# Kernel optimization log

Hardware: AMD Instinct MI355X
Metric: run time of the kernel (lower is better)

## Reference

```python
import jax, jax.numpy as jnp
import numpy as np

B, D, H, U, K = 256, 512, 512, 24, 8
IK, IV, NIH = 64, 400, 1          # input attention: key/query 64, value 400, 1 head
CK, CQ, NCH = 32, 32, 4           # comm attention: key/query 32, 4 heads
CV = H                            # comm_value_size forced to hidden_size in __init__
_SQ_IK = np.float32(np.sqrt(IK))
_SQ_CK = np.float32(np.sqrt(CK))


def setup_inputs() -> dict:
    key = jax.random.key(0)
    ks = jax.random.split(key, 12)
    n = jax.random.normal
    s = jnp.float32(0.02)
    return {
        "x": n(ks[0], (B, 1, D), jnp.float32),
        "hs": n(ks[1], (B, U, H), jnp.float32),
        "cs": n(ks[2], (B, U, H), jnp.float32),
        "key_w": n(ks[3], (D, NIH * IK)) * s,
        "key_b": jnp.zeros((NIH * IK,), jnp.float32),
        "value_w": n(ks[4], (D, NIH * IV)) * s,
        "value_b": jnp.zeros((NIH * IV,), jnp.float32),
        "query_w": n(ks[5], (U, H, NIH * IK)) * s,
        "i2h_w": n(ks[6], (U, IV, 4 * H)) * s,
        "h2h_w": n(ks[7], (U, H, 4 * H)) * s,
        "qc_w": n(ks[8], (U, H, NCH * CQ)) * s,
        "kc_w": n(ks[9], (U, H, NCH * CK)) * s,
        "vc_w": n(ks[10], (U, H, NCH * CV)) * s,
        "co_w": n(ks[11], (U, NCH * CV, CV)) * s,
    }


def _forward(x, hs, cs, key_w, key_b, value_w, value_b, query_w,
             i2h_w, h2h_w, qc_w, kc_w, vc_w, co_w):
    b = x.shape[0]
    # append null input -> [B,2,D]
    xx = jnp.concatenate([x, jnp.zeros_like(x)], axis=1)
    # ---- input attention + top-k unit selection ----
    k_lay = (xx @ key_w + key_b).reshape(b, 2, NIH, IK).transpose(0, 2, 1, 3)    # [B,NIH,2,IK]
    v_lay = (xx @ value_w + value_b).reshape(b, 2, NIH, IV).mean(axis=2)         # [B,2,IV] (mean over heads)
    q_lay = jnp.einsum('buh,uhk->buk', hs, query_w).reshape(b, U, NIH, IK).transpose(0, 2, 1, 3)
    scores = jnp.einsum('bnuk,bntk->bnut', q_lay, k_lay) / _SQ_IK               # [B,NIH,U,2]
    scores = scores.mean(axis=1)                                                 # [B,U,2]
    _, idx = jax.lax.top_k(scores[:, :, 0], K)                                   # top-k on not-null score
    mask = jnp.zeros((b, U), x.dtype).at[jnp.arange(b)[:, None], idx].set(1.0)   # [B,U]
    probs = jax.nn.softmax(scores, axis=-1)                                      # dropout off (eval)
    inp = jnp.einsum('but,btv->buv', probs, v_lay) * mask[:, :, None]            # [B,U,IV]
    # ---- block LSTM (GroupLSTMCell) ----
    preact = (jnp.einsum('buv,uvh->buh', inp, i2h_w)
              + jnp.einsum('buh,uhg->bug', hs, h2h_w))                           # [B,U,4H]
    i_t = jax.nn.sigmoid(preact[..., :H])
    f_t = jax.nn.sigmoid(preact[..., H:2 * H])
    o_t = jax.nn.sigmoid(preact[..., 2 * H:3 * H])
    g_t = jnp.tanh(preact[..., 3 * H:])
    c_t = cs * f_t + i_t * g_t
    h_t = o_t * jnp.tanh(c_t)
    m3 = mask[:, :, None]
    # blocked_grad: identity forward, grad*mask backward
    h_blk = h_t * m3 + jax.lax.stop_gradient(h_t * (1.0 - m3))
    # ---- multi-head communication attention ----
    qc = jnp.einsum('buh,uhk->buk', h_blk, qc_w).reshape(b, U, NCH, CQ).transpose(0, 2, 1, 3)
    kc = jnp.einsum('buh,uhk->buk', h_blk, kc_w).reshape(b, U, NCH, CK).transpose(0, 2, 1, 3)
    vc = jnp.einsum('buh,uhk->buk', h_blk, vc_w).reshape(b, U, NCH, CV).transpose(0, 2, 1, 3)
    att = jax.nn.softmax(jnp.einsum('bnuk,bntk->bnut', qc, kc) / _SQ_CK, axis=-1)
    att = att * mask[:, None, :, None]                                           # mask query rows
    ctx = jnp.einsum('bnut,bntv->bnuv', att, vc).transpose(0, 2, 1, 3).reshape(b, U, NCH * CV)
    ctx = jnp.einsum('bud,udh->buh', ctx, co_w) + h_blk
    # ---- masked state update ----
    hs_new = m3 * ctx + (1.0 - m3) * hs
    cs_new = m3 * c_t + (1.0 - m3) * cs
    return hs_new, cs_new


def reference(x, hs, cs, key_w, key_b, value_w, value_b, query_w,
              i2h_w, h2h_w, qc_w, kc_w, vc_w, co_w):
    return _forward(x, hs, cs, key_w, key_b, value_w, value_b, query_w,
                    i2h_w, h2h_w, qc_w, kc_w, vc_w, co_w)
```

## Files before the change

### kernel.cpp

```cpp
#include <hip/hip_runtime.h>


typedef unsigned short u16;
typedef __bf16 bf16_t;
typedef bf16_t bf16x8 __attribute__((ext_vector_type(8)));
typedef float f32x16 __attribute__((ext_vector_type(16)));

union V8 { uint4 u; bf16x8 v; u16 us[8]; };

__device__ __forceinline__ float u2f(u16 u) {
    union { unsigned int i; float f; } c; c.i = ((unsigned int)u) << 16; return c.f;
}
__device__ __forceinline__ u16 f2u(float f) {
    union { bf16_t b; u16 u; } c; c.b = (bf16_t)f; return c.u;
}

__global__ __launch_bounds__(256) void kv_kernel(
    const float* __restrict__ x, const float* __restrict__ key_w, const float* __restrict__ key_b,
    const float* __restrict__ value_w, const float* __restrict__ value_b,
    float* __restrict__ k0, float* __restrict__ v0)
{
    __shared__ float xs[512];
    const int b = blockIdx.x, tid = threadIdx.x;
    for (int i = tid; i < 512; i += 256) xs[i] = x[b * 512 + i];
    __syncthreads();
    if (tid < 64) {
        float acc = 0.f;
        for (int d = 0; d < 512; ++d) acc += xs[d] * key_w[d * 64 + tid];
        k0[b * 64 + tid] = acc + key_b[tid];
    }
    for (int v = tid; v < 400; v += 256) {
        float acc = 0.f;
        for (int d = 0; d < 512; ++d) acc += xs[d] * value_w[d * 400 + v];
        v0[b * 400 + v] = acc + value_b[v];
    }
}

__global__ __launch_bounds__(64) void qscore_kernel(
    const float* __restrict__ hs, const float* __restrict__ query_w,
    const float* __restrict__ k0, const float* __restrict__ key_b,
    float* __restrict__ scores)
{
    __shared__ float hsu[512];
    const int u = blockIdx.x, b = blockIdx.y, lane = threadIdx.x;
    const float* h = hs + ((size_t)(b * 24 + u)) * 512;
    for (int i = lane; i < 512; i += 64) hsu[i] = h[i];
    __syncthreads();
    const float* qw = query_w + (size_t)u * 512 * 64 + lane;
    float q = 0.f;
    for (int d = 0; d < 512; ++d) q += hsu[d] * qw[(size_t)d * 64];
    float p0 = q * k0[b * 64 + lane];
    float p1 = q * key_b[lane];
    #pragma unroll
    for (int off = 32; off > 0; off >>= 1) {
        p0 += __shfl_down(p0, off);
        p1 += __shfl_down(p1, off);
    }
    if (lane == 0) {
        scores[(b * 24 + u) * 2 + 0] = p0 * 0.125f;
        scores[(b * 24 + u) * 2 + 1] = p1 * 0.125f;
    }
}

__global__ __launch_bounds__(64) void topk_kernel(
    const float* __restrict__ scores, float* __restrict__ mask, float* __restrict__ probs)
{
    __shared__ float s0[24];
    const int b = blockIdx.x, tid = threadIdx.x;
    if (tid < 24) s0[tid] = scores[(b * 24 + tid) * 2];
    __syncthreads();
    if (tid < 24) {
        const float su = s0[tid];
        int rank = 0;
        for (int t = 0; t < 24; ++t) {
            float st = s0[t];
            rank += (st > su) || (st == su && t < tid);
        }
        mask[b * 24 + tid] = (rank < 8) ? 1.f : 0.f;
        const float a = su, c = scores[(b * 24 + tid) * 2 + 1];
        const float m = fmaxf(a, c);
        const float e0 = expf(a - m), e1 = expf(c - m);
        const float inv = 1.f / (e0 + e1);
        probs[(b * 24 + tid) * 2 + 0] = e0 * inv;
        probs[(b * 24 + tid) * 2 + 1] = e1 * inv;
    }
}

__global__ __launch_bounds__(256) void inp_kernel(
    const float* __restrict__ probs, const float* __restrict__ v0,
    const float* __restrict__ value_b, const float* __restrict__ mask,
    u16* __restrict__ inp)
{
    const int idx = blockIdx.x * 256 + threadIdx.x;
    const int v = idx % 416, bu = idx / 416, b = bu / 24;
    float val = 0.f;
    if (v < 400)
        val = (probs[bu * 2] * v0[b * 400 + v] + probs[bu * 2 + 1] * value_b[v]) * mask[bu];
    inp[idx] = f2u(val);
}

__global__ __launch_bounds__(256) void tobf16_kernel(
    const float* __restrict__ src, u16* __restrict__ dst)
{
    const int idx = blockIdx.x * 256 + threadIdx.x;
    dst[idx] = f2u(src[idx]);
}

__device__ __forceinline__ void gemm_pipe(
    const u16* __restrict__ aB1, int lda1,
    const float* __restrict__ bB1, int ldb1, int K1, int ns1,
    const u16* __restrict__ aB2, int lda2,
    const float* __restrict__ bB2, int ldb2, int K2, int ns2,
    int ar, int ac, int bn, int bkg, int wm, int wn, int fr, int kh,
    u16* __restrict__ As0, u16* __restrict__ As1,
    u16* __restrict__ Bs0, u16* __restrict__ Bs1,
    f32x16 acc[2][2])
{
    const int nst = ns1 + ns2;
    uint4 a0A, a1A, a0B, a1B;
    float rbA[16], rbB[16];

    auto issue = [&](int t, uint4& x0, uint4& x1, float* rb) {
        const bool s2 = (t >= ns1);
        const int k0 = (s2 ? t - ns1 : t) << 5;
        const int lda = s2 ? lda2 : lda1;
        const int ldb = s2 ? ldb2 : ldb1;
        const int K   = s2 ? K2 : K1;
        const u16* ap = (s2 ? aB2 : aB1) + k0;
        x0 = *(const uint4*)ap;
        x1 = *(const uint4*)(ap + (size_t)64 * lda);
        const float* bp = (s2 ? bB2 : bB1) + (size_t)k0 * ldb;
        if (k0 + 32 <= K) {
            #pragma unroll
            for (int j = 0; j < 16; ++j) rb[j] = bp[(size_t)j * ldb];
        } else {
            #pragma unroll
            for (int j = 0; j < 16; ++j)
                rb[j] = (k0 + bkg + j < K) ? bp[(size_t)j * ldb] : 0.f;
        }
    };

    auto convstore = [&](const uint4& x0, const uint4& x1, const float* rb,
                         u16* __restrict__ As, u16* __restrict__ Bs) {
        *(uint4*)&As[ar * 40 + ac]        = x0;
        *(uint4*)&As[(ar + 64) * 40 + ac] = x1;
        V8 lo, hi;
        #pragma unroll
        for (int j = 0; j < 8; ++j) lo.us[j] = f2u(rb[j]);
        #pragma unroll
        for (int j = 0; j < 8; ++j) hi.us[j] = f2u(rb[8 + j]);
        *(uint4*)&Bs[bn * 40 + bkg]     = lo.u;
        *(uint4*)&Bs[bn * 40 + bkg + 8] = hi.u;
    };

    auto compute = [&](const u16* __restrict__ As, const u16* __restrict__ Bs) {
        #pragma unroll
        for (int kk = 0; kk < 32; kk += 16) {
            V8 a0, a1, b0, b1;
            a0.u = *(const uint4*)&As[(wm + fr) * 40 + kk + kh];
            a1.u = *(const uint4*)&As[(wm + 32 + fr) * 40 + kk + kh];
            b0.u = *(const uint4*)&Bs[(wn + fr) * 40 + kk + kh];
            b1.u = *(const uint4*)&Bs[(wn + 32 + fr) * 40 + kk + kh];
            acc[0][0] = __builtin_amdgcn_mfma_f32_32x32x16_bf16(a0.v, b0.v, acc[0][0], 0, 0, 0);
            acc[0][1] = __builtin_amdgcn_mfma_f32_32x32x16_bf16(a0.v, b1.v, acc[0][1], 0, 0, 0);
            acc[1][0] = __builtin_amdgcn_mfma_f32_32x32x16_bf16(a1.v, b0.v, acc[1][0], 0, 0, 0);
            acc[1][1] = __builtin_amdgcn_mfma_f32_32x32x16_bf16(a1.v, b1.v, acc[1][1], 0, 0, 0);
        }
    };

    issue(0, a0A, a1A, rbA);
    convstore(a0A, a1A, rbA, As0, Bs0);
    if (nst > 1) issue(1, a0B, a1B, rbB);
    __syncthreads();

    for (int t = 0; t < nst; t += 2) {
        compute(As0, Bs0);
        if (t + 1 < nst) convstore(a0B, a1B, rbB, As1, Bs1);
        if (t + 2 < nst) issue(t + 2, a0A, a1A, rbA);
        __syncthreads();
        if (t + 1 < nst) {
            compute(As1, Bs1);
            if (t + 2 < nst) convstore(a0A, a1A, rbA, As0, Bs0);
            if (t + 3 < nst) issue(t + 3, a0B, a1B, rbB);
            __syncthreads();
        }
    }
}

__global__ __launch_bounds__(256, 2) void mfma_gemm(
    const u16* __restrict__ A1, int lda1, int aus1,
    const float* __restrict__ B1, int ldb1, int bus1, int K1,
    const u16* __restrict__ A2, int lda2, int aus2,
    const float* __restrict__ B2, int ldb2, int bus2, int K2,
    void* __restrict__ Cv, int ldc, int cus, int mode,
    int skA, int skB, int skC)
{
    __shared__ __align__(16) u16 As[2][128 * 40];
    __shared__ __align__(16) u16 Bs[2][128 * 40];
    const int u = blockIdx.z;
    const int n0 = blockIdx.x * 128;
    const int mb = blockIdx.y & 1, sk = blockIdx.y >> 1;
    const int m0 = mb * 128;
    const int tid = threadIdx.x;
    const int ar = tid >> 2, ac = (tid & 3) * 8;
    const int bn = tid & 127, bkg = (tid >> 7) * 16;
    const int w = tid >> 6, lane = tid & 63;
    const int wm = (w >> 1) * 64, wn = (w & 1) * 64;
    const int fr = lane & 31, kh = (lane >> 5) * 8;

    const int ns1 = (K1 + 31) >> 5;
    const int ns2 = K2 ? (K2 + 31) >> 5 : 0;

    const u16* aB1 = A1 + (size_t)sk * skA + (size_t)u * aus1 + (size_t)(m0 + ar) * lda1 + ac;
    const float* bB1 = B1 + (size_t)sk * skB + (size_t)u * bus1 + (size_t)bkg * ldb1 + n0 + bn;
    const u16* aB2 = aB1; const float* bB2 = bB1; int lda2e = lda1, ldb2e = ldb1;
    if (K2) {
        aB2 = A2 + (size_t)u * aus2 + (size_t)(m0 + ar) * lda2 + ac;
        bB2 = B2 + (size_t)u * bus2 + (size_t)bkg * ldb2 + n0 + bn;
        lda2e = lda2; ldb2e = ldb2;
    }

    f32x16 acc[2][2];
    #pragma unroll
    for (int i = 0; i < 2; ++i)
        #pragma unroll
        for (int j = 0; j < 2; ++j)
            #pragma unroll
            for (int r = 0; r < 16; ++r) acc[i][j][r] = 0.f;

    gemm_pipe(aB1, lda1, bB1, ldb1, K1, ns1,
              aB2, lda2e, bB2, ldb2e, K2, ns2,
              ar, ac, bn, bkg, wm, wn, fr, kh,
              As[0], As[1], Bs[0], Bs[1], acc);

    const size_t skoff = (size_t)sk * (size_t)skC;
    const int rbase = (lane >> 5) * 4;
    #pragma unroll
    for (int i = 0; i < 2; ++i) {
        #pragma unroll
        for (int j = 0; j < 2; ++j) {
            const int gn = n0 + wn + j * 32 + fr;
            #pragma unroll
            for (int r = 0; r < 16; ++r) {
                const int row = (r & 3) + 8 * (r >> 2) + rbase;
                const int gm = m0 + wm + i * 32 + row;
                const size_t idx = (size_t)u * cus + (size_t)gm * ldc + gn + skoff;
                if (mode == 0) ((float*)Cv)[idx] = acc[i][j][r];
                else           ((u16*)Cv)[idx]  = f2u(acc[i][j][r]);
            }
        }
    }
}

__global__ __launch_bounds__(256, 2) void mfma_gemm_kqv(
    const u16* __restrict__ ht,
    const float* __restrict__ kc_w, const float* __restrict__ qc_w, const float* __restrict__ vc_w,
    u16* __restrict__ kc, u16* __restrict__ qcb, u16* __restrict__ vc)
{
    __shared__ __align__(16) u16 As[2][128 * 40];
    __shared__ __align__(16) u16 Bs[2][128 * 40];
    const int u = blockIdx.z;
    const int bx = blockIdx.x;
    const int m0 = blockIdx.y * 128;
    const int tid = threadIdx.x;
    const int ar = tid >> 2, ac = (tid & 3) * 8;
    const int bn = tid & 127, bkg = (tid >> 7) * 16;
    const int w = tid >> 6, lane = tid & 63;
    const int wm = (w >> 1) * 64, wn = (w & 1) * 64;
    const int fr = lane & 31, kh = (lane >> 5) * 8;

    const float* Bw; u16* Cd; int ldb, bus, n0, ldc, cus;
    if (bx == 0)      { Bw = kc_w; Cd = kc;  ldb = 128;  bus = 512 * 128;  n0 = 0;              ldc = 3072;  cus = 128;  }
    else if (bx == 1) { Bw = qc_w; Cd = qcb; ldb = 128;  bus = 512 * 128;  n0 = 0;              ldc = 3072;  cus = 128;  }
    else              { Bw = vc_w; Cd = vc;  ldb = 2048; bus = 512 * 2048; n0 = (bx - 2) * 128; ldc = 49152; cus = 2048; }

    const u16* aB = ht + (size_t)u * 512 + (size_t)(m0 + ar) * 12288 + ac;
    const float* bB = Bw + (size_t)u * bus + (size_t)bkg * ldb + n0 + bn;

    f32x16 acc[2][2];
    #pragma unroll
    for (int i = 0; i < 2; ++i)
        #pragma unroll
        for (int j = 0; j < 2; ++j)
            #pragma unroll
            for (int r = 0; r < 16; ++r) acc[i][j][r] = 0.f;

    gemm_pipe(aB, 12288, bB, ldb, 512, 16,
              aB, 12288, bB, ldb, 0, 0,
              ar, ac, bn, bkg, wm, wn, fr, kh,
              As[0], As[1], Bs[0], Bs[1], acc);

    const int rbase = (lane >> 5) * 4;
    #pragma unroll
    for (int i = 0; i < 2; ++i) {
        #pragma unroll
        for (int j = 0; j < 2; ++j) {
            const int gn = n0 + wn + j * 32 + fr;
            #pragma unroll
            for (int r = 0; r < 16; ++r) {
                const int row = (r & 3) + 8 * (r >> 2) + rbase;
                const int gm = m0 + wm + i * 32 + row;
                Cd[(size_t)u * cus + (size_t)gm * ldc + gn] = f2u(acc[i][j][r]);
            }
        }
    }
}

__global__ __launch_bounds__(256) void gates_kernel(
    const float* __restrict__ preact, const float* __restrict__ cs,
    const float* __restrict__ mask,
    u16* __restrict__ ht, float* __restrict__ out_cs)
{
    const int idx = blockIdx.x * 256 + threadIdx.x;
    const int h = idx & 511, bu = idx >> 9;
    const float* pre = preact + (size_t)bu * 2048;
    const float it = 1.f / (1.f + expf(-pre[h]));
    const float ft = 1.f / (1.f + expf(-pre[512 + h]));
    const float ot = 1.f / (1.f + expf(-pre[1024 + h]));
    const float gt = tanhf(pre[1536 + h]);
    const float c = cs[idx] * ft + it * gt;
    ht[idx] = f2u(ot * tanhf(c));
    out_cs[idx] = (mask[bu] != 0.f) ? c : cs[idx];
}

__global__ __launch_bounds__(64) void attn_kernel(
    const u16* __restrict__ qc, const u16* __restrict__ kc, const u16* __restrict__ vc,
    const float* __restrict__ mask, u16* __restrict__ ctx)
{
    const int u = blockIdx.x, nc = blockIdx.y, b = blockIdx.z;
    if (mask[b * 24 + u] == 0.f) return;
    const int lane = threadIdx.x;
    __shared__ float kcs[24][32];
    __shared__ float qv[32];
    __shared__ float ss[24];
    __shared__ float ps[24];
    for (int i = lane; i < 24 * 32; i += 64) {
        const int t = i >> 5, k = i & 31;
        kcs[t][k] = u2f(kc[((size_t)(b * 24 + t)) * 128 + nc * 32 + k]);
    }
    if (lane < 32) qv[lane] = u2f(qc[((size_t)(b * 24 + u)) * 128 + nc * 32 + lane]);
    __syncthreads();
    if (lane < 24) {
        float s = 0.f;
        for (int k = 0; k < 32; ++k) s += qv[k] * kcs[lane][k];
        ss[lane] = s * 0.17677669529663687f;
    }
    __syncthreads();
    float m = -1e30f;
    for (int t = 0; t < 24; ++t) m = fmaxf(m, ss[t]);
    float sum = 0.f;
    for (int t = 0; t < 24; ++t) sum += expf(ss[t] - m);
    const float inv = 1.f / sum;
    if (lane < 24) ps[lane] = expf(ss[lane] - m) * inv;
    __syncthreads();
    float acc[8] = {};
    const u16* vcb = vc + (size_t)b * 24 * 2048 + nc * 512 + lane;
    for (int t = 0; t < 24; ++t) {
        const float pt = ps[t];
        const u16* vr = vcb + (size_t)t * 2048;
        #pragma unroll
        for (int j = 0; j < 8; ++j) acc[j] += pt * u2f(vr[j * 64]);
    }
    u16* cb = ctx + ((size_t)(b * 24 + u)) * 2048 + nc * 512 + lane;
    #pragma unroll
    for (int j = 0; j < 8; ++j) cb[j * 64] = f2u(acc[j]);
}

__global__ __launch_bounds__(256) void co_reduce(
    const float* __restrict__ p, const float* __restrict__ mask,
    const u16* __restrict__ ht, const float* __restrict__ hs,
    float* __restrict__ out_hs)
{
    const int idx = blockIdx.x * 256 + threadIdx.x;
    const int bu = idx >> 9;
    out_hs[idx] = (mask[bu] != 0.f)
        ? (p[idx] + p[idx + 6144 * 512] + u2f(ht[idx]))
        : hs[idx];
}

extern "C" void kernel_launch(void* const* d_in, const int* in_sizes, int n_in,
                              void* d_out, int out_size, void* d_ws, size_t ws_size,
                              hipStream_t stream)
{
    (void)in_sizes; (void)n_in; (void)out_size; (void)ws_size;
    const float* x       = (const float*)d_in[0];
    const float* hs      = (const float*)d_in[1];
    const float* cs      = (const float*)d_in[2];
    const float* key_w   = (const float*)d_in[3];
    const float* key_b   = (const float*)d_in[4];
    const float* value_w = (const float*)d_in[5];
    const float* value_b = (const float*)d_in[6];
    const float* query_w = (const float*)d_in[7];
    const float* i2h_w   = (const float*)d_in[8];
    const float* h2h_w   = (const float*)d_in[9];
    const float* qc_w    = (const float*)d_in[10];
    const float* kc_w    = (const float*)d_in[11];
    const float* vc_w    = (const float*)d_in[12];
    const float* co_w    = (const float*)d_in[13];

    char* ws = (char*)d_ws;
    float* k0     = (float*)(ws + 0);
    float* v0     = (float*)(ws + 65536);
    float* scores = (float*)(ws + 475136);
    float* probs  = (float*)(ws + 524288);
    float* mask   = (float*)(ws + 573440);
    u16*   inp    = (u16*)  (ws + 598016);
    float* preact = (float*)(ws + 5709824);
    u16*   vc     = (u16*)  (ws + 5709824);
    float* co_p   = (float*)(ws + 5709824);
    u16*   ctx    = (u16*)  (ws + 30875648);
    u16*   ht     = (u16*)  (ws + 56041472);
    u16*   kc     = (u16*)  (ws + 62332928);
    u16*   qcb    = (u16*)  (ws + 63905792);
    u16*   hsb    = (u16*)  (ws + 65478656);

    float* out_hs = (float*)d_out;
    float* out_cs = out_hs + (size_t)256 * 24 * 512;

    kv_kernel<<<256, 256, 0, stream>>>(x, key_w, key_b, value_w, value_b, k0, v0);
    qscore_kernel<<<dim3(24, 256), 64, 0, stream>>>(hs, query_w, k0, key_b, scores);
    topk_kernel<<<256, 64, 0, stream>>>(scores, mask, probs);
    inp_kernel<<<(256 * 24 * 416) / 256, 256, 0, stream>>>(probs, v0, value_b, mask, inp);
    tobf16_kernel<<<(256 * 24 * 512) / 256, 256, 0, stream>>>(hs, hsb);

    mfma_gemm<<<dim3(16, 2, 24), 256, 0, stream>>>(
        inp, 9984, 416, i2h_w, 2048, 400 * 2048, 400,
        hsb, 12288, 512, h2h_w, 2048, 512 * 2048, 512,
        preact, 49152, 2048, 0, 0, 0, 0);

    gates_kernel<<<12288, 256, 0, stream>>>(preact, cs, mask, ht, out_cs);

    mfma_gemm_kqv<<<dim3(18, 2, 24), 256, 0, stream>>>(ht, kc_w, qc_w, vc_w, kc, qcb, vc);

    attn_kernel<<<dim3(24, 4, 256), 64, 0, stream>>>(qcb, kc, vc, mask, ctx);

    mfma_gemm<<<dim3(4, 4, 24), 256, 0, stream>>>(
        ctx, 49152, 2048, co_w, 512, 2048 * 512, 1024,
        nullptr, 0, 0, nullptr, 0, 0, 0,
        co_p, 12288, 512, 0, 1024, 1024 * 512, 6144 * 512);

    co_reduce<<<12288, 256, 0, stream>>>(co_p, mask, ht, hs, out_hs);
}
```

Before: 651.3 us.

## Deepen GEMM prefetch, fuse hs bf16 conversion, widen kv and attention blocks

The GEMM mainloop now issues global loads two stages ahead and replaces __syncthreads with a barrier that waits only on LDS counters, so global prefetches can stay in flight across barriers. The hs-to-bf16 conversion moves into qscore_kernel, which removes a separate elementwise launch and one extra pass over hs. kv_kernel uses 512 threads so each key/value column has its own thread, and attn_kernel packs the four heads into one 256-thread block, cutting block count and the masked-out early-exit launches. The custom barrier relies on s_waitcnt lgkmcnt(0) alone being enough for LDS visibility, and the extra in-flight loads raise register pressure.

```diff
diff --git a/kernel.cpp b/kernel.cpp
--- a/kernel.cpp
+++ b/kernel.cpp
@@ -15,21 +15,25 @@
     union { bf16_t b; u16 u; } c; c.b = (bf16_t)f; return c.u;
 }
 
-__global__ __launch_bounds__(256) void kv_kernel(
+__device__ __forceinline__ void bar_lds() {
+    asm volatile("s_waitcnt lgkmcnt(0)\n\ts_barrier" ::: "memory");
+}
+
+__global__ __launch_bounds__(512) void kv_kernel(
     const float* __restrict__ x, const float* __restrict__ key_w, const float* __restrict__ key_b,
     const float* __restrict__ value_w, const float* __restrict__ value_b,
     float* __restrict__ k0, float* __restrict__ v0)
 {
     __shared__ float xs[512];
     const int b = blockIdx.x, tid = threadIdx.x;
-    for (int i = tid; i < 512; i += 256) xs[i] = x[b * 512 + i];
+    xs[tid] = x[b * 512 + tid];
     __syncthreads();
     if (tid < 64) {
         float acc = 0.f;
         for (int d = 0; d < 512; ++d) acc += xs[d] * key_w[d * 64 + tid];
         k0[b * 64 + tid] = acc + key_b[tid];
-    }
-    for (int v = tid; v < 400; v += 256) {
+    } else if (tid < 464) {
+        const int v = tid - 64;
         float acc = 0.f;
         for (int d = 0; d < 512; ++d) acc += xs[d] * value_w[d * 400 + v];
         v0[b * 400 + v] = acc + value_b[v];
@@ -39,12 +43,17 @@
 __global__ __launch_bounds__(64) void qscore_kernel(
     const float* __restrict__ hs, const float* __restrict__ query_w,
     const float* __restrict__ k0, const float* __restrict__ key_b,
-    float* __restrict__ scores)
+    float* __restrict__ scores, u16* __restrict__ hsb)
 {
     __shared__ float hsu[512];
     const int u = blockIdx.x, b = blockIdx.y, lane = threadIdx.x;
-    const float* h = hs + ((size_t)(b * 24 + u)) * 512;
-    for (int i = lane; i < 512; i += 64) hsu[i] = h[i];
+    const size_t base = ((size_t)(b * 24 + u)) * 512;
+    const float* h = hs + base;
+    for (int i = lane; i < 512; i += 64) {
+        const float v = h[i];
+        hsu[i] = v;
+        hsb[base + i] = f2u(v);
+    }
     __syncthreads();
     const float* qw = query_w + (size_t)u * 512 * 64 + lane;
     float q = 0.f;
@@ -99,13 +108,6 @@
     inp[idx] = f2u(val);
 }
 
-__global__ __launch_bounds__(256) void tobf16_kernel(
-    const float* __restrict__ src, u16* __restrict__ dst)
-{
-    const int idx = blockIdx.x * 256 + threadIdx.x;
-    dst[idx] = f2u(src[idx]);
-}
-
 __device__ __forceinline__ void gemm_pipe(
     const u16* __restrict__ aB1, int lda1,
     const float* __restrict__ bB1, int ldb1, int K1, int ns1,
@@ -169,22 +171,23 @@
     };
 
     issue(0, a0A, a1A, rbA);
+    if (nst > 1) issue(1, a0B, a1B, rbB);
     convstore(a0A, a1A, rbA, As0, Bs0);
-    if (nst > 1) issue(1, a0B, a1B, rbB);
-    __syncthreads();
-
-    for (int t = 0; t < nst; t += 2) {
+    if (nst > 2) issue(2, a0A, a1A, rbA);
+    bar_lds();
+
+    int t = 0;
+    for (; t + 2 <= nst; t += 2) {
         compute(As0, Bs0);
-        if (t + 1 < nst) convstore(a0B, a1B, rbB, As1, Bs1);
-        if (t + 2 < nst) issue(t + 2, a0A, a1A, rbA);
-        __syncthreads();
-        if (t + 1 < nst) {
-            compute(As1, Bs1);
-            if (t + 2 < nst) convstore(a0A, a1A, rbA, As0, Bs0);
-            if (t + 3 < nst) issue(t + 3, a0B, a1B, rbB);
-            __syncthreads();
-        }
-    }
+        convstore(a0B, a1B, rbB, As1, Bs1);
+        if (t + 3 < nst) issue(t + 3, a0B, a1B, rbB);
+        bar_lds();
+        compute(As1, Bs1);
+        if (t + 2 < nst) convstore(a0A, a1A, rbA, As0, Bs0);
+        if (t + 4 < nst) issue(t + 4, a0A, a1A, rbA);
+        bar_lds();
+    }
+    if (t < nst) compute(As0, Bs0);
 }
 
 __global__ __launch_bounds__(256, 2) void mfma_gemm(
@@ -323,40 +326,40 @@
     out_cs[idx] = (mask[bu] != 0.f) ? c : cs[idx];
 }
 
-__global__ __launch_bounds__(64) void attn_kernel(
+__global__ __launch_bounds__(256) void attn_kernel(
     const u16* __restrict__ qc, const u16* __restrict__ kc, const u16* __restrict__ vc,
     const float* __restrict__ mask, u16* __restrict__ ctx)
 {
-    const int u = blockIdx.x, nc = blockIdx.y, b = blockIdx.z;
+    const int u = blockIdx.x, b = blockIdx.y;
     if (mask[b * 24 + u] == 0.f) return;
-    const int lane = threadIdx.x;
-    __shared__ float kcs[24][32];
-    __shared__ float qv[32];
-    __shared__ float ss[24];
-    __shared__ float ps[24];
+    const int nc = threadIdx.x >> 6, lane = threadIdx.x & 63;
+    __shared__ float kcs[4][24][32];
+    __shared__ float qv[4][32];
+    __shared__ float ss[4][24];
+    __shared__ float ps[4][24];
     for (int i = lane; i < 24 * 32; i += 64) {
         const int t = i >> 5, k = i & 31;
-        kcs[t][k] = u2f(kc[((size_t)(b * 24 + t)) * 128 + nc * 32 + k]);
-    }
-    if (lane < 32) qv[lane] = u2f(qc[((size_t)(b * 24 + u)) * 128 + nc * 32 + lane]);
+        kcs[nc][t][k] = u2f(kc[((size_t)(b * 24 + t)) * 128 + nc * 32 + k]);
+    }
+    if (lane < 32) qv[nc][lane] = u2f(qc[((size_t)(b * 24 + u)) * 128 + nc * 32 + lane]);
     __syncthreads();
     if (lane < 24) {
         float s = 0.f;
-        for (int k = 0; k < 32; ++k) s += qv[k] * kcs[lane][k];
-        ss[lane] = s * 0.17677669529663687f;
+        for (int k = 0; k < 32; ++k) s += qv[nc][k] * kcs[nc][lane][k];
+        ss[nc][lane] = s * 0.17677669529663687f;
     }
     __syncthreads();
     float m = -1e30f;
-    for (int t = 0; t < 24; ++t) m = fmaxf(m, ss[t]);
+    for (int t = 0; t < 24; ++t) m = fmaxf(m, ss[nc][t]);
     float sum = 0.f;
-    for (int t = 0; t < 24; ++t) sum += expf(ss[t] - m);
+    for (int t = 0; t < 24; ++t) sum += expf(ss[nc][t] - m);
     const float inv = 1.f / sum;
-    if (lane < 24) ps[lane] = expf(ss[lane] - m) * inv;
+    if (lane < 24) ps[nc][lane] = expf(ss[nc][lane] - m) * inv;
     __syncthreads();
     float acc[8] = {};
     const u16* vcb = vc + (size_t)b * 24 * 2048 + nc * 512 + lane;
     for (int t = 0; t < 24; ++t) {
-        const float pt = ps[t];
+        const float pt = ps[nc][t];
         const u16* vr = vcb + (size_t)t * 2048;
         #pragma unroll
         for (int j = 0; j < 8; ++j) acc[j] += pt * u2f(vr[j * 64]);
@@ -417,11 +420,10 @@
     float* out_hs = (float*)d_out;
     float* out_cs = out_hs + (size_t)256 * 24 * 512;
 
-    kv_kernel<<<256, 256, 0, stream>>>(x, key_w, key_b, value_w, value_b, k0, v0);
-    qscore_kernel<<<dim3(24, 256), 64, 0, stream>>>(hs, query_w, k0, key_b, scores);
+    kv_kernel<<<256, 512, 0, stream>>>(x, key_w, key_b, value_w, value_b, k0, v0);
+    qscore_kernel<<<dim3(24, 256), 64, 0, stream>>>(hs, query_w, k0, key_b, scores, hsb);
     topk_kernel<<<256, 64, 0, stream>>>(scores, mask, probs);
     inp_kernel<<<(256 * 24 * 416) / 256, 256, 0, stream>>>(probs, v0, value_b, mask, inp);
-    tobf16_kernel<<<(256 * 24 * 512) / 256, 256, 0, stream>>>(hs, hsb);
 
     mfma_gemm<<<dim3(16, 2, 24), 256, 0, stream>>>(
         inp, 9984, 416, i2h_w, 2048, 400 * 2048, 400,
@@ -432,7 +434,7 @@
 
     mfma_gemm_kqv<<<dim3(18, 2, 24), 256, 0, stream>>>(ht, kc_w, qc_w, vc_w, kc, qcb, vc);
 
-    attn_kernel<<<dim3(24, 4, 256), 64, 0, stream>>>(qcb, kc, vc, mask, ctx);
+    attn_kernel<<<dim3(24, 256), 256, 0, stream>>>(qcb, kc, vc, mask, ctx);
 
     mfma_gemm<<<dim3(4, 4, 24), 256, 0, stream>>>(
         ctx, 49152, 2048, co_w, 512, 2048 * 512, 1024,
```

After: 594.8 us. -8.7%, faster.
